# Kernel tuning notes

Measured on AMD Instinct MI355X. Metric: run time of the kernel, lower is better.

## Reference

```python
import jax, jax.numpy as jnp
import numpy as np

B, N, D = 8, 2048, 256      # batch, tokens, model dim (= out_token_dims)
S = 128                     # query_key_dims
H = int(2.0 * D)            # expansion_factor * D = 512
EPS = 1e-5


def setup_inputs() -> dict:
    key = jax.random.key(0)
    ks = jax.random.split(key, 4)
    x = jax.random.normal(ks[0], (B, N, D), dtype=jnp.float32)
    g = jnp.ones((), jnp.float32)                                # ScaleNorm gain
    W_uv = jax.random.normal(ks[1], (D, 2 * H + S), jnp.float32) * 0.02
    b_uv = jnp.zeros((2 * H + S,), jnp.float32)
    gamma = jnp.ones((2, S), jnp.float32)                        # OffsetScale scale
    beta = jnp.zeros((2, S), jnp.float32)                        # OffsetScale offset
    W_o = jax.random.normal(ks[2], (H, D), jnp.float32) * 0.02
    b_o = jnp.zeros((D,), jnp.float32)
    return {"x": x, "g": g, "W_uv": W_uv, "b_uv": b_uv,
            "gamma": gamma, "beta": beta, "W_o": W_o, "b_o": b_o}


def reference(x, g, W_uv, b_uv, gamma, beta, W_o, b_o):
    d = x.shape[-1]
    # ScaleNorm: x / max(||x|| / sqrt(d), eps) * g
    norm = jnp.linalg.norm(x, axis=-1, keepdims=True) * jax.lax.rsqrt(jnp.float32(d))
    xn = x / jnp.maximum(norm, EPS) * g
    # fused uv projection + SiLU
    uv = jax.nn.silu(jnp.einsum('bnd,de->bne', xn, W_uv) + b_uv)
    u = uv[..., :H]            # gate branch        [B,N,H]
    v = uv[..., H:2 * H]       # value branch       [B,N,H]
    base = uv[..., 2 * H:]     # shared q/k base    [B,N,S]
    # OffsetScale heads=2 -> q, k (cheap per-dim affine)
    q = base * gamma[0] + beta[0]
    k = base * gamma[1] + beta[1]
    # single-head scores + ReLU^2 attention activation
    qk = jnp.einsum('bns,bms->bnm', q, k) * jax.lax.rsqrt(jnp.float32(S))
    attn = jnp.square(jax.nn.relu(qk))
    # gate * (attn @ v), then output projection back to D
    gated = u * jnp.einsum('bnm,bmh->bnh', attn, v)
    return jnp.einsum('bnh,hd->bnd', gated, W_o) + b_o
```

## Files before the change

kernel.cpp:

```cpp
#include <hip/hip_runtime.h>
#include <math.h>

#define BB 8
#define NN 2048
#define DD 256
#define SS 128
#define HH 512
#define EE 1152

typedef short bf16x8 __attribute__((ext_vector_type(8)));
typedef float f32x4 __attribute__((ext_vector_type(4)));

__device__ __forceinline__ short f2bf(float f) {
    union { float f; unsigned u; } a; a.f = f;
    unsigned r = a.u + 0x7FFFu + ((a.u >> 16) & 1u);
    return (short)(r >> 16);
}
__device__ __forceinline__ float bf2f(short s) {
    union { unsigned u; float f; } a; a.u = ((unsigned)(unsigned short)s) << 16;
    return a.f;
}

__global__ __launch_bounds__(256) void k_pre(
        const float* __restrict__ x, const float* __restrict__ gp,
        short* __restrict__ xn,
        const float* __restrict__ Wuv, const float* __restrict__ Wo,
        short* __restrict__ Wuv_t, short* __restrict__ Wo_t) {
    __shared__ float tile[32][33];
    int bid = blockIdx.x;
    int t = threadIdx.x;
    if (bid < 4096) {
        int wave = t >> 6, lane = t & 63;
        long row = (long)bid * 4 + wave;
        float4 xv = ((const float4*)(x + row * DD))[lane];
        float ss = xv.x*xv.x + xv.y*xv.y + xv.z*xv.z + xv.w*xv.w;
        #pragma unroll
        for (int off = 32; off > 0; off >>= 1) ss += __shfl_down(ss, off);
        ss = __shfl(ss, 0);
        float norm = sqrtf(ss) * 0.0625f;
        float scale = gp[0] / fmaxf(norm, 1e-5f);
        short4 o;
        o.x = f2bf(xv.x * scale); o.y = f2bf(xv.y * scale);
        o.z = f2bf(xv.z * scale); o.w = f2bf(xv.w * scale);
        ((short4*)(xn + row * DD))[lane] = o;
    } else if (bid < 4384) {
        int bid2 = bid - 4096;
        int et = bid2 % 36, dt = bid2 / 36;
        #pragma unroll
        for (int i = 0; i < 4; i++) {
            int idx = t + i*256, r = idx >> 5, c = idx & 31;
            tile[r][c] = Wuv[(long)(dt*32 + r)*EE + et*32 + c];
        }
        __syncthreads();
        #pragma unroll
        for (int i = 0; i < 4; i++) {
            int idx = t + i*256, r = idx >> 5, c = idx & 31;
            Wuv_t[(long)(et*32 + r)*DD + dt*32 + c] = f2bf(tile[c][r]);
        }
    } else {
        int bid3 = bid - 4384;
        int ht = bid3 % 16, dt = bid3 / 16;
        #pragma unroll
        for (int i = 0; i < 4; i++) {
            int idx = t + i*256, r = idx >> 5, c = idx & 31;
            tile[r][c] = Wo[(long)(ht*32 + r)*DD + dt*32 + c];
        }
        __syncthreads();
        #pragma unroll
        for (int i = 0; i < 4; i++) {
            int idx = t + i*256, r = idx >> 5, c = idx & 31;
            Wo_t[(long)(dt*32 + r)*HH + ht*32 + c] = f2bf(tile[c][r]);
        }
    }
}

__global__ __launch_bounds__(256, 3) void k_gemm1(
        const short* __restrict__ xn, const short* __restrict__ Wuv_t,
        const float* __restrict__ b_uv,
        const float* __restrict__ gamma, const float* __restrict__ beta,
        short* __restrict__ u, short* __restrict__ vfrag,
        short* __restrict__ q, short* __restrict__ k) {
    __shared__ short As[128*64];
    __shared__ short Bs[128*64];
    int m0 = blockIdx.x * 128, n0 = blockIdx.y * 128;
    int t = threadIdx.x, w = t >> 6, lane = t & 63;
    int wr = w & 1, wc = w >> 1, l16 = lane & 15, quad = lane >> 4;
    int srow = t >> 1, scol = (t & 1) * 32;
    f32x4 acc[4][4] = {};
    bf16x8 aS[4], bS[4];
    #pragma unroll
    for (int j = 0; j < 4; j++) {
        aS[j] = *(const bf16x8*)&xn[(long)(m0 + srow)*DD + scol + j*8];
        bS[j] = *(const bf16x8*)&Wuv_t[(long)(n0 + srow)*DD + scol + j*8];
    }
    for (int ki = 0; ki < 4; ki++) {
        #pragma unroll
        for (int j = 0; j < 4; j++) {
            *(bf16x8*)&As[srow*64 + scol + j*8] = aS[j];
            *(bf16x8*)&Bs[srow*64 + scol + j*8] = bS[j];
        }
        __syncthreads();
        if (ki < 3) {
            int k0 = (ki + 1) * 64;
            #pragma unroll
            for (int j = 0; j < 4; j++) {
                aS[j] = *(const bf16x8*)&xn[(long)(m0 + srow)*DD + k0 + scol + j*8];
                bS[j] = *(const bf16x8*)&Wuv_t[(long)(n0 + srow)*DD + k0 + scol + j*8];
            }
        }
        #pragma unroll
        for (int kk = 0; kk < 2; kk++) {
            bf16x8 a[4], bb[4];
            #pragma unroll
            for (int mt = 0; mt < 4; mt++)
                a[mt] = *(const bf16x8*)&As[(wr*64 + mt*16 + l16)*64 + kk*32 + quad*8];
            #pragma unroll
            for (int nt = 0; nt < 4; nt++)
                bb[nt] = *(const bf16x8*)&Bs[(wc*64 + nt*16 + l16)*64 + kk*32 + quad*8];
            #pragma unroll
            for (int mt = 0; mt < 4; mt++)
                #pragma unroll
                for (int nt = 0; nt < 4; nt++)
                    acc[mt][nt] = __builtin_amdgcn_mfma_f32_16x16x32_bf16(
                        a[mt], bb[nt], acc[mt][nt], 0,0,0);
        }
        __syncthreads();
    }
    #pragma unroll
    for (int mt = 0; mt < 4; mt++)
    #pragma unroll
    for (int nt = 0; nt < 4; nt++) {
        int gm0 = m0 + wr*64 + mt*16 + quad*4;
        int ge  = n0 + wc*64 + nt*16 + l16;
        float val[4];
        #pragma unroll
        for (int r = 0; r < 4; r++) {
            float xv = acc[mt][nt][r] + b_uv[ge];
            val[r] = xv / (1.0f + __expf(-xv));
        }
        if (ge < HH) {
            #pragma unroll
            for (int r = 0; r < 4; r++)
                u[(long)(gm0 + r)*HH + ge] = f2bf(val[r]);
        } else if (ge < 2*HH) {
            int h = ge - HH;
            long base = (((long)((gm0 >> 11)*64 + ((gm0 & 2047) >> 5)) * 32)
                         + (h >> 4)) * 512
                        + ((((gm0 & 31) >> 3)*16 + (h & 15)) * 8) + (gm0 & 7);
            short4 o;
            o.x = f2bf(val[0]); o.y = f2bf(val[1]);
            o.z = f2bf(val[2]); o.w = f2bf(val[3]);
            *(short4*)&vfrag[base] = o;
        } else {
            int si = ge - 2*HH;
            #pragma unroll
            for (int r = 0; r < 4; r++) {
                q[(long)(gm0 + r)*SS + si] = f2bf(val[r] * gamma[si]      + beta[si]);
                k[(long)(gm0 + r)*SS + si] = f2bf(val[r] * gamma[SS + si] + beta[SS + si]);
            }
        }
    }
}

#define KS(p,row)  (smem + ((p)*32 + (row))*136)
#define PS(p,row)  (smem + 8704 + ((p)*64 + (row))*40)
#define GT(hf,row) (smem + (hf)*16896 + (row)*264)

__global__ __launch_bounds__(512, 2) void k_attn(
        const short* __restrict__ q, const short* __restrict__ k,
        const short* __restrict__ vfrag, const short* __restrict__ u,
        const short* __restrict__ Wo_t, const float* __restrict__ b_o,
        float* __restrict__ out) {
    extern __shared__ __align__(16) short smem[];
    int b = blockIdx.x & 7;
    int i0 = (blockIdx.x >> 3) * 64;
    int t = threadIdx.x, w = t >> 6, lane = t & 63;
    int l16 = lane & 15, quad = lane >> 4;
    int qt = w >> 1, mt = w & 1;
    const short* qb  = q + ((long)b * NN + i0) * SS;
    const short* kb  = k + (long)b * NN * SS;
    const short* vfb = vfrag + (long)b * 64 * 32 * 512;
    const float RS = 0.08838834764831845f;

    int krow = t >> 4, kch = (t & 15) * 8;

    bf16x8 qf[4];
    #pragma unroll
    for (int kc = 0; kc < 4; kc++)
        qf[kc] = *(const bf16x8*)&qb[(long)(qt*16 + l16)*SS + kc*32 + quad*8];

    *(bf16x8*)&KS(0,krow)[kch] = *(const bf16x8*)&kb[(long)krow*SS + kch];
    bf16x8 kregB = *(const bf16x8*)&kb[(long)(32 + krow)*SS + kch];
    bf16x8 kregA = *(const bf16x8*)&kb[(long)(64 + krow)*SS + kch];
    bf16x8 vfA[4], vfB[4];
    #pragma unroll
    for (int jj = 0; jj < 4; jj++)
        vfA[jj] = *(const bf16x8*)&vfb[((long)(w*4 + jj))*512 + lane*8];
    __syncthreads();

    f32x4 acc[16] = {};
    for (int s = 0; s < 32; s++) {
        {
            f32x4 sc = {};
            #pragma unroll
            for (int kc = 0; kc < 4; kc++) {
                bf16x8 kf = *(const bf16x8*)&KS(0, mt*16 + l16)[kc*32 + quad*8];
                sc = __builtin_amdgcn_mfma_f32_16x16x32_bf16(kf, qf[kc], sc, 0,0,0);
            }
            short4 pw;
            float s0 = fmaxf(sc[0]*RS, 0.f), s1 = fmaxf(sc[1]*RS, 0.f);
            float s2 = fmaxf(sc[2]*RS, 0.f), s3 = fmaxf(sc[3]*RS, 0.f);
            pw.x = f2bf(s0*s0); pw.y = f2bf(s1*s1);
            pw.z = f2bf(s2*s2); pw.w = f2bf(s3*s3);
            *(short4*)&PS(0, qt*16 + l16)[mt*16 + quad*4] = pw;
            *(bf16x8*)&KS(1, krow)[kch] = kregB;
            __syncthreads();
            int tk = (2*s + 3 < 64) ? 2*s + 3 : 63;
            kregB = *(const bf16x8*)&kb[(long)(tk*32 + krow)*SS + kch];
            #pragma unroll
            for (int jj = 0; jj < 4; jj++)
                vfB[jj] = *(const bf16x8*)&vfb[((long)(2*s+1)*32 + w*4 + jj)*512 + lane*8];
            bf16x8 af[4];
            #pragma unroll
            for (int qq2 = 0; qq2 < 4; qq2++)
                af[qq2] = *(const bf16x8*)&PS(0, qq2*16 + l16)[quad*8];
            #pragma unroll
            for (int jj = 0; jj < 4; jj++)
                #pragma unroll
                for (int qq2 = 0; qq2 < 4; qq2++)
                    acc[qq2*4 + jj] = __builtin_amdgcn_mfma_f32_16x16x32_bf16(
                        af[qq2], vfA[jj], acc[qq2*4 + jj], 0,0,0);
        }
        {
            f32x4 sc = {};
            #pragma unroll
            for (int kc = 0; kc < 4; kc++) {
                bf16x8 kf = *(const bf16x8*)&KS(1, mt*16 + l16)[kc*32 + quad*8];
                sc = __builtin_amdgcn_mfma_f32_16x16x32_bf16(kf, qf[kc], sc, 0,0,0);
            }
            short4 pw;
            float s0 = fmaxf(sc[0]*RS, 0.f), s1 = fmaxf(sc[1]*RS, 0.f);
            float s2 = fmaxf(sc[2]*RS, 0.f), s3 = fmaxf(sc[3]*RS, 0.f);
            pw.x = f2bf(s0*s0); pw.y = f2bf(s1*s1);
            pw.z = f2bf(s2*s2); pw.w = f2bf(s3*s3);
            *(short4*)&PS(1, qt*16 + l16)[mt*16 + quad*4] = pw;
            *(bf16x8*)&KS(0, krow)[kch] = kregA;
            __syncthreads();
            int tk = (2*s + 4 < 64) ? 2*s + 4 : 63;
            kregA = *(const bf16x8*)&kb[(long)(tk*32 + krow)*SS + kch];
            int tv = (2*s + 2 < 64) ? 2*s + 2 : 63;
            #pragma unroll
            for (int jj = 0; jj < 4; jj++)
                vfA[jj] = *(const bf16x8*)&vfb[((long)tv*32 + w*4 + jj)*512 + lane*8];
            bf16x8 af[4];
            #pragma unroll
            for (int qq2 = 0; qq2 < 4; qq2++)
                af[qq2] = *(const bf16x8*)&PS(1, qq2*16 + l16)[quad*8];
            #pragma unroll
            for (int jj = 0; jj < 4; jj++)
                #pragma unroll
                for (int qq2 = 0; qq2 < 4; qq2++)
                    acc[qq2*4 + jj] = __builtin_amdgcn_mfma_f32_16x16x32_bf16(
                        af[qq2], vfB[jj], acc[qq2*4 + jj], 0,0,0);
        }
    }

    long rowbase = (long)b * NN + i0;
    __syncthreads();
    {
        int hf = w >> 2;
        int hbase = (w & 3) * 64;
        #pragma unroll
        for (int qq2 = 0; qq2 < 4; qq2++)
        #pragma unroll
        for (int jj = 0; jj < 4; jj++) {
            int gh = w*64 + jj*16 + l16;
            #pragma unroll
            for (int r = 0; r < 4; r++) {
                long grow = rowbase + qq2*16 + quad*4 + r;
                float uval = bf2f(u[grow*HH + gh]);
                GT(hf, qq2*16 + quad*4 + r)[hbase + jj*16 + l16] =
                    f2bf(acc[qq2*4 + jj][r] * uval);
            }
        }
    }
    __syncthreads();
    f32x4 acc2[4][2] = {};
    #pragma unroll
    for (int p = 0; p < 2; p++) {
        #pragma unroll
        for (int kc = 0; kc < 8; kc++) {
            bf16x8 A[4], Bf[2];
            #pragma unroll
            for (int mt2 = 0; mt2 < 4; mt2++)
                A[mt2] = *(const bf16x8*)&GT(p, mt2*16 + l16)[kc*32 + quad*8];
            #pragma unroll
            for (int nt = 0; nt < 2; nt++)
                Bf[nt] = *(const bf16x8*)&Wo_t[(long)(w*32 + nt*16 + l16)*HH
                                               + p*256 + kc*32 + quad*8];
            #pragma unroll
            for (int mt2 = 0; mt2 < 4; mt2++)
                #pragma unroll
                for (int nt = 0; nt < 2; nt++)
                    acc2[mt2][nt] = __builtin_amdgcn_mfma_f32_16x16x32_bf16(
                        A[mt2], Bf[nt], acc2[mt2][nt], 0,0,0);
        }
    }
    #pragma unroll
    for (int mt2 = 0; mt2 < 4; mt2++)
    #pragma unroll
    for (int nt = 0; nt < 2; nt++)
    #pragma unroll
    for (int r = 0; r < 4; r++) {
        long grow = rowbase + mt2*16 + quad*4 + r;
        int gd = w*32 + nt*16 + l16;
        out[grow*DD + gd] = acc2[mt2][nt][r] + b_o[gd];
    }
}

extern "C" void kernel_launch(void* const* d_in, const int* in_sizes, int n_in,
                              void* d_out, int out_size, void* d_ws, size_t ws_size,
                              hipStream_t stream) {
    const float* x     = (const float*)d_in[0];
    const float* g     = (const float*)d_in[1];
    const float* Wuv   = (const float*)d_in[2];
    const float* b_uv  = (const float*)d_in[3];
    const float* gamma = (const float*)d_in[4];
    const float* beta  = (const float*)d_in[5];
    const float* Wo    = (const float*)d_in[6];
    const float* b_o   = (const float*)d_in[7];
    float* out = (float*)d_out;

    short* ws    = (short*)d_ws;
    short* xn    = ws;
    short* Wuv_t = xn    + (long)16384 * 256;
    short* Wo_t  = Wuv_t + (long)1152 * 256;
    short* u     = Wo_t  + (long)256 * 512;
    short* vfrag = u     + (long)16384 * 512;
    short* qq    = vfrag + (long)16384 * 512;
    short* kk    = qq    + (long)16384 * 128;

    k_pre<<<4512, 256, 0, stream>>>(x, g, xn, Wuv, Wo, Wuv_t, Wo_t);
    k_gemm1<<<dim3(128, 9), 256, 0, stream>>>(xn, Wuv_t, b_uv, gamma, beta,
                                              u, vfrag, qq, kk);
    k_attn<<<256, 512, 67584, stream>>>(qq, kk, vfrag, u, Wo_t, b_o, out);
}
```

Before: 172.2 us.

## Use direct global-to-LDS loads and LDS-staged coalesced epilogue in uv GEMM

Replaces the register-staged prefetch of A/B tiles in the uv projection GEMM with global_load_lds direct-to-LDS transfers. This drops the software double buffering, so loads are no longer overlapped with MFMA work. The epilogue now writes SiLU results as bf16 into an LDS transpose tile, then emits wide vectorized stores for u, vfrag and q/k. Those stores replace the scattered per-element 2-byte writes. Shared memory grows to 34 KB dynamic and the launch-bounds occupancy hint is removed, which may reduce occupancy.

```diff
diff --git a/kernel.cpp b/kernel.cpp
--- a/kernel.cpp
+++ b/kernel.cpp
@@ -19,6 +19,11 @@
 __device__ __forceinline__ float bf2f(short s) {
     union { unsigned u; float f; } a; a.u = ((unsigned)(unsigned short)s) << 16;
     return a.f;
+}
+__device__ __forceinline__ void gl_lds16(const short* g, short* l) {
+    __builtin_amdgcn_global_load_lds(
+        (const __attribute__((address_space(1))) void*)g,
+        (__attribute__((address_space(3))) void*)l, 16, 0, 0);
 }
 
 __global__ __launch_bounds__(256) void k_pre(
@@ -74,49 +79,39 @@
     }
 }
 
-__global__ __launch_bounds__(256, 3) void k_gemm1(
+#define AS1(i) (smem1 + (i))
+#define BS1(i) (smem1 + 8192 + (i))
+#define TT(r)  (smem1 + (r)*136)
+__global__ __launch_bounds__(256) void k_gemm1(
         const short* __restrict__ xn, const short* __restrict__ Wuv_t,
         const float* __restrict__ b_uv,
         const float* __restrict__ gamma, const float* __restrict__ beta,
         short* __restrict__ u, short* __restrict__ vfrag,
         short* __restrict__ q, short* __restrict__ k) {
-    __shared__ short As[128*64];
-    __shared__ short Bs[128*64];
+    extern __shared__ __align__(16) short smem1[];
     int m0 = blockIdx.x * 128, n0 = blockIdx.y * 128;
     int t = threadIdx.x, w = t >> 6, lane = t & 63;
     int wr = w & 1, wc = w >> 1, l16 = lane & 15, quad = lane >> 4;
-    int srow = t >> 1, scol = (t & 1) * 32;
+    int lr = lane >> 3, lc = (lane & 7) * 8;
     f32x4 acc[4][4] = {};
-    bf16x8 aS[4], bS[4];
-    #pragma unroll
-    for (int j = 0; j < 4; j++) {
-        aS[j] = *(const bf16x8*)&xn[(long)(m0 + srow)*DD + scol + j*8];
-        bS[j] = *(const bf16x8*)&Wuv_t[(long)(n0 + srow)*DD + scol + j*8];
-    }
-    for (int ki = 0; ki < 4; ki++) {
-        #pragma unroll
-        for (int j = 0; j < 4; j++) {
-            *(bf16x8*)&As[srow*64 + scol + j*8] = aS[j];
-            *(bf16x8*)&Bs[srow*64 + scol + j*8] = bS[j];
-        }
+    for (int k0 = 0; k0 < DD; k0 += 64) {
         __syncthreads();
-        if (ki < 3) {
-            int k0 = (ki + 1) * 64;
-            #pragma unroll
-            for (int j = 0; j < 4; j++) {
-                aS[j] = *(const bf16x8*)&xn[(long)(m0 + srow)*DD + k0 + scol + j*8];
-                bS[j] = *(const bf16x8*)&Wuv_t[(long)(n0 + srow)*DD + k0 + scol + j*8];
-            }
-        }
+        #pragma unroll
+        for (int i = 0; i < 4; i++) {
+            int r0 = i*32 + w*8;
+            gl_lds16(&xn[(long)(m0 + r0 + lr)*DD + k0 + lc], AS1(r0*64));
+            gl_lds16(&Wuv_t[(long)(n0 + r0 + lr)*DD + k0 + lc], BS1(r0*64));
+        }
+        __syncthreads();
         #pragma unroll
         for (int kk = 0; kk < 2; kk++) {
             bf16x8 a[4], bb[4];
             #pragma unroll
             for (int mt = 0; mt < 4; mt++)
-                a[mt] = *(const bf16x8*)&As[(wr*64 + mt*16 + l16)*64 + kk*32 + quad*8];
+                a[mt] = *(const bf16x8*)AS1((wr*64 + mt*16 + l16)*64 + kk*32 + quad*8);
             #pragma unroll
             for (int nt = 0; nt < 4; nt++)
-                bb[nt] = *(const bf16x8*)&Bs[(wc*64 + nt*16 + l16)*64 + kk*32 + quad*8];
+                bb[nt] = *(const bf16x8*)BS1((wc*64 + nt*16 + l16)*64 + kk*32 + quad*8);
             #pragma unroll
             for (int mt = 0; mt < 4; mt++)
                 #pragma unroll
@@ -124,40 +119,59 @@
                     acc[mt][nt] = __builtin_amdgcn_mfma_f32_16x16x32_bf16(
                         a[mt], bb[nt], acc[mt][nt], 0,0,0);
         }
-        __syncthreads();
-    }
+    }
+    __syncthreads();
     #pragma unroll
     for (int mt = 0; mt < 4; mt++)
     #pragma unroll
     for (int nt = 0; nt < 4; nt++) {
-        int gm0 = m0 + wr*64 + mt*16 + quad*4;
-        int ge  = n0 + wc*64 + nt*16 + l16;
-        float val[4];
+        int col = wc*64 + nt*16 + l16;
+        float bias = b_uv[n0 + col];
         #pragma unroll
         for (int r = 0; r < 4; r++) {
-            float xv = acc[mt][nt][r] + b_uv[ge];
-            val[r] = xv / (1.0f + __expf(-xv));
-        }
-        if (ge < HH) {
-            #pragma unroll
-            for (int r = 0; r < 4; r++)
-                u[(long)(gm0 + r)*HH + ge] = f2bf(val[r]);
-        } else if (ge < 2*HH) {
-            int h = ge - HH;
-            long base = (((long)((gm0 >> 11)*64 + ((gm0 & 2047) >> 5)) * 32)
-                         + (h >> 4)) * 512
-                        + ((((gm0 & 31) >> 3)*16 + (h & 15)) * 8) + (gm0 & 7);
-            short4 o;
-            o.x = f2bf(val[0]); o.y = f2bf(val[1]);
-            o.z = f2bf(val[2]); o.w = f2bf(val[3]);
-            *(short4*)&vfrag[base] = o;
-        } else {
-            int si = ge - 2*HH;
-            #pragma unroll
-            for (int r = 0; r < 4; r++) {
-                q[(long)(gm0 + r)*SS + si] = f2bf(val[r] * gamma[si]      + beta[si]);
-                k[(long)(gm0 + r)*SS + si] = f2bf(val[r] * gamma[SS + si] + beta[SS + si]);
+            int row = wr*64 + mt*16 + quad*4 + r;
+            float xv = acc[mt][nt][r] + bias;
+            TT(row)[col] = f2bf(xv / (1.0f + __expf(-xv)));
+        }
+    }
+    __syncthreads();
+    if (n0 < 512) {
+        int row = t >> 1, ch = (t & 1) * 64;
+        long gm = m0 + row;
+        #pragma unroll
+        for (int j = 0; j < 8; j++)
+            *(bf16x8*)&u[gm*HH + n0 + ch + j*8] = *(const bf16x8*)&TT(row)[ch + j*8];
+    } else if (n0 < 1024) {
+        int h0 = n0 - 512;
+        int f = t >> 3, sub = t & 7;
+        int mtl = f >> 3, htl = f & 7;
+        long fbase = (((long)((m0 >> 11)*64 + ((m0 & 2047) >> 5) + mtl) * 32)
+                      + (h0 >> 4) + htl) * 512;
+        #pragma unroll
+        for (int i = 0; i < 8; i++) {
+            int l = sub*8 + i, qv = l >> 4, l16v = l & 15;
+            bf16x8 o;
+            #pragma unroll
+            for (int e = 0; e < 8; e++)
+                o[e] = TT(mtl*32 + qv*8 + e)[htl*16 + l16v];
+            *(bf16x8*)&vfrag[fbase + (long)l*8] = o;
+        }
+    } else {
+        int row = t >> 1, ch = (t & 1) * 64;
+        long gm = m0 + row;
+        #pragma unroll
+        for (int j = 0; j < 8; j++) {
+            bf16x8 a = *(const bf16x8*)&TT(row)[ch + j*8];
+            bf16x8 oq, ok;
+            #pragma unroll
+            for (int e = 0; e < 8; e++) {
+                int si = ch + j*8 + e;
+                float val = bf2f(a[e]);
+                oq[e] = f2bf(val * gamma[si]      + beta[si]);
+                ok[e] = f2bf(val * gamma[SS + si] + beta[SS + si]);
             }
+            *(bf16x8*)&q[gm*SS + ch + j*8] = oq;
+            *(bf16x8*)&k[gm*SS + ch + j*8] = ok;
         }
     }
 }
@@ -341,7 +355,7 @@
     short* kk    = qq    + (long)16384 * 128;
 
     k_pre<<<4512, 256, 0, stream>>>(x, g, xn, Wuv, Wo, Wuv_t, Wo_t);
-    k_gemm1<<<dim3(128, 9), 256, 0, stream>>>(xn, Wuv_t, b_uv, gamma, beta,
-                                              u, vfrag, qq, kk);
+    k_gemm1<<<dim3(128, 9), 256, 34816, stream>>>(xn, Wuv_t, b_uv, gamma, beta,
+                                                  u, vfrag, qq, kk);
     k_attn<<<256, 512, 67584, stream>>>(qq, kk, vfrag, u, Wo_t, b_o, out);
 }
```

Result: slower. 182.5 us (+6.0%).
